# Performance work log

Measured on AMD Instinct MI355X. Metric: run time of the kernel, lower is better.

## Reference

```python
import jax, jax.numpy as jnp
import numpy as np
from jax import lax

B, C, H, W = 4, 64, 128, 128
G, K, CO = 8, 3, 64
KK = K * K
MC = G * KK  # mask channels = 72


def _conv3x3(x, w, b):
    # standard 3x3 conv, stride 1, padding 1, NCHW
    y = lax.conv_general_dilated(x, w, (1, 1), ((1, 1), (1, 1)),
                                 dimension_numbers=('NCHW', 'OIHW', 'NCHW'))
    return y + b[None, :, None, None]


def _deform_conv2d(x, offset, mask, w, b):
    """Modulated deformable conv (DCNv2), stride=1, padding=1, dilation=1.
    offset: [B, 2*G*KK, H, W] interpreted as [B, G, KK, 2(dy,dx), H, W] (torchvision layout).
    mask:   [B, G*KK, H, W].
    w: [Co, C/G, K, K], b: [Co].
    """
    Bn, Cn, Hn, Wn = x.shape
    Co, Cg, Kh, Kw = w.shape
    Gn = Cn // Cg
    KKn = Kh * Kw
    Ho, Wo = Hn, Wn  # stride 1, pad 1, k 3

    off = offset.reshape(Bn, Gn, KKn, 2, Ho, Wo)
    dy, dx = off[:, :, :, 0], off[:, :, :, 1]
    m = mask.reshape(Bn, Gn, 1, KKn, Ho, Wo)

    kh = (jnp.arange(KKn) // Kw).astype(x.dtype)  # kernel row index
    kw = (jnp.arange(KKn) % Kw).astype(x.dtype)
    hh = jnp.arange(Ho, dtype=x.dtype)
    ww = jnp.arange(Wo, dtype=x.dtype)
    # sampling positions: h - pad + kh*dil + dy  -> [B,G,KK,Ho,Wo]
    py = hh[None, None, None, :, None] - 1.0 + kh[None, None, :, None, None] + dy
    px = ww[None, None, None, None, :] - 1.0 + kw[None, None, :, None, None] + dx

    y0 = jnp.floor(py); x0 = jnp.floor(px)
    ly = py - y0; lx = px - x0
    y0i = y0.astype(jnp.int32); x0i = x0.astype(jnp.int32)
    y1i = y0i + 1; x1i = x0i + 1

    xg = x.reshape(Bn, Gn, Cg, Hn * Wn)

    def corner(yi, xi, wgt):
        valid = ((yi >= 0) & (yi < Hn) & (xi >= 0) & (xi < Wn)).astype(x.dtype)
        idx = (jnp.clip(yi, 0, Hn - 1) * Wn + jnp.clip(xi, 0, Wn - 1))
        idx = idx.reshape(Bn, Gn, 1, KKn * Ho * Wo)
        v = jnp.take_along_axis(xg, idx, axis=3).reshape(Bn, Gn, Cg, KKn, Ho, Wo)
        return v * (wgt * valid)[:, :, None]

    val = (corner(y0i, x0i, (1.0 - ly) * (1.0 - lx))
           + corner(y0i, x1i, (1.0 - ly) * lx)
           + corner(y1i, x0i, ly * (1.0 - lx))
           + corner(y1i, x1i, ly * lx))
    val = val * m  # modulation

    wr = w.reshape(Gn, Co // Gn, Cg, KKn)
    out = jnp.einsum('bgckhw,gock->bgohw', val, wr).reshape(Bn, Co, Ho, Wo)
    return out + b[None, :, None, None]


def setup_inputs() -> dict:
    key = jax.random.key(0)
    ks = jax.random.split(key, 8)
    f = lambda k, s, sc=1.0: jax.random.normal(k, s, dtype=jnp.float32) * sc
    return {
        'x': f(ks[0], (B, C, H, W)),
        'share_with_feat': f(ks[1], (B, C, H, W)),
        'offset_feat': f(ks[2], (B, C, H, W)),
        # conv_offset_mask: C -> 3*G*KK (zero-init in original; small random here)
        'w_om': f(ks[3], (3 * MC, C, 3, 3), 0.02),
        'b_om': jnp.zeros((3 * MC,), jnp.float32),
        'w_em1': f(ks[4], (C, 2 * C, 3, 3), 0.05),
        'b_em1': jnp.zeros((C,), jnp.float32),
        'w_em2': f(ks[5], (MC, C, 3, 3), 0.05),
        'b_em2': jnp.zeros((MC,), jnp.float32),
        # deform conv weight: [Co, C/G, 3, 3]
        'w_dc': f(ks[6], (CO, C // G, 3, 3), 0.05),
        'b_dc': f(ks[7], (CO,), 0.05),
    }


def reference(x, share_with_feat, offset_feat, w_om, b_om, w_em1, b_em1,
              w_em2, b_em2, w_dc, b_dc):
    om = _conv3x3(offset_feat, w_om, b_om)
    o1, o2, mask_x = jnp.split(om, 3, axis=1)
    offset = jnp.concatenate([o1, o2], axis=1)
    mask_x = jax.nn.sigmoid(mask_x)
    x_deform = _deform_conv2d(x, offset, mask_x, w_dc, b_dc)
    # extra_mask=True branch
    em = _conv3x3(jnp.concatenate([share_with_feat, offset_feat], axis=1), w_em1, b_em1)
    em = jnp.where(em >= 0, em, 0.1 * em)  # LeakyReLU(0.1)
    em = jax.nn.sigmoid(_conv3x3(em, w_em2, b_em2))
    share_deform = _deform_conv2d(share_with_feat, offset, em, w_dc, b_dc)
    return (x_deform, share_deform)
```

## Files before the change

kernel.cpp:

```cpp
#include <hip/hip_runtime.h>
#include <math.h>

#define BB 4
#define CC 64
#define HH 128
#define WW 128
#define GG 8
#define COO 64
#define HWC (HH*WW)

#define DPAD 12
#define DROW 26

typedef float f32x16 __attribute__((ext_vector_type(16)));
typedef __bf16 bf16x8 __attribute__((ext_vector_type(8)));

__device__ __forceinline__ unsigned short bf16_rn(float f) {
    unsigned int u = __float_as_uint(f);
    unsigned int r = (u + 0x7fffu + ((u >> 16) & 1u)) >> 16;
    return (unsigned short)r;
}
__device__ __forceinline__ float b2f(unsigned short u) {
    return __uint_as_float(((unsigned int)u) << 16);
}

__global__ __launch_bounds__(256) void pack_inputs_kernel(
    const float* __restrict__ x, const float* __restrict__ share,
    const float* __restrict__ offf,
    unsigned int* __restrict__ xs, unsigned short* __restrict__ sc16,
    unsigned short* __restrict__ oc16)
{
    __shared__ unsigned short lds[64][66];
    const int b = blockIdx.y;
    const int pix0 = blockIdx.x * 64;
    const int t = threadIdx.x;
    const int p = t & 63, q = t >> 6;
    const int pl = t & 63, cg = t >> 6;

#pragma unroll
    for (int i = 0; i < 16; i++) {
        int c = i * 4 + q;
        size_t idx = ((size_t)b * 64 + c) * HWC + pix0 + p;
        unsigned short sb = bf16_rn(share[idx]);
        lds[c][p] = sb;
        xs[idx] = (unsigned int)bf16_rn(x[idx]) | ((unsigned int)sb << 16);
    }
    __syncthreads();
    {
        unsigned int u[8];
#pragma unroll
        for (int j = 0; j < 8; j++) {
            unsigned int lo = lds[cg * 16 + 2 * j][pl];
            unsigned int hi = lds[cg * 16 + 2 * j + 1][pl];
            u[j] = lo | (hi << 16);
        }
        unsigned int* dst = (unsigned int*)(sc16 + ((size_t)(b * 4 + cg) * HWC + pix0 + pl) * 16);
        *(uint4*)dst = make_uint4(u[0], u[1], u[2], u[3]);
        *(uint4*)(dst + 4) = make_uint4(u[4], u[5], u[6], u[7]);
    }
    __syncthreads();

#pragma unroll
    for (int i = 0; i < 16; i++) {
        int c = i * 4 + q;
        lds[c][p] = bf16_rn(offf[((size_t)b * 64 + c) * HWC + pix0 + p]);
    }
    __syncthreads();
    {
        unsigned int u[8];
#pragma unroll
        for (int j = 0; j < 8; j++) {
            unsigned int lo = lds[cg * 16 + 2 * j][pl];
            unsigned int hi = lds[cg * 16 + 2 * j + 1][pl];
            u[j] = lo | (hi << 16);
        }
        unsigned int* dst = (unsigned int*)(oc16 + ((size_t)(b * 4 + cg) * HWC + pix0 + pl) * 16);
        *(uint4*)dst = make_uint4(u[0], u[1], u[2], u[3]);
        *(uint4*)(dst + 4) = make_uint4(u[4], u[5], u[6], u[7]);
    }
}

__device__ __forceinline__ void pack_w_one(const float* __restrict__ w,
                                           unsigned short* __restrict__ wp,
                                           int Cout, int COP, int CinTot, int idx) {
    int i  = idx & 15;
    int co = (idx >> 4) % COP;
    int t  = idx / (16 * COP);
    int cg = t & 3;
    int kk = (t >> 2) % 9;
    int seg = t / 36;
    int cin = seg * 64 + cg * 16 + i;
    float v = (co < Cout) ? w[((size_t)co * CinTot + cin) * 9 + kk] : 0.f;
    wp[idx] = bf16_rn(v);
}

__global__ void pack_w_all_kernel(const float* __restrict__ w_om, unsigned short* __restrict__ wp_om,
                                  const float* __restrict__ w_em1, unsigned short* __restrict__ wp_em1,
                                  const float* __restrict__ w_em2, unsigned short* __restrict__ wp_em2) {
    int i = blockIdx.x * 256 + threadIdx.x;
    if (i < 129024) {
        pack_w_one(w_om, wp_om, 216, 224, 64, i);
    } else if (i < 129024 + 73728) {
        pack_w_one(w_em1, wp_em1, 64, 64, 128, i - 129024);
    } else if (i < 129024 + 73728 + 55296) {
        pack_w_one(w_em2, wp_em2, 72, 96, 64, i - 129024 - 73728);
    }
}

template<int NSEG, int NT>
__global__ __launch_bounds__(256) void conv_mfma_kernel(
    const unsigned short* __restrict__ in0,
    const unsigned short* __restrict__ in1,
    const unsigned short* __restrict__ wp,
    const float* __restrict__ bias,
    void* __restrict__ out,
    int Cout, int COP, int out_mode, int act)
{
    constexpr int XS = 128 / (NT * 32);
    const int lane = threadIdx.x & 63;
    const int wid  = threadIdx.x >> 6;
    const int l31  = lane & 31;
    const int half = lane >> 5;
    int tmp = blockIdx.x;
    const int xsp = tmp % XS; tmp /= XS;
    const int rb  = tmp % (HH / 4);
    const int b   = tmp / (HH / 4);
    const int r   = rb * 4 + wid;
    const int px0 = xsp * NT * 32;
    const int co0 = blockIdx.y * 32;

    f32x16 acc[NT];
#pragma unroll
    for (int nt = 0; nt < NT; nt++)
#pragma unroll
        for (int rg = 0; rg < 16; rg++) acc[nt][rg] = 0.f;

    bf16x8 bz;
#pragma unroll
    for (int i = 0; i < 8; i++) bz[i] = (__bf16)0.f;

#pragma unroll
    for (int seg = 0; seg < NSEG; seg++) {
        const unsigned short* in = seg ? in1 : in0;
        const unsigned short* inb = in + (size_t)b * 4 * HWC * 16;
#pragma unroll
        for (int kk = 0; kk < 9; kk++) {
            const int rr = r + kk / 3 - 1;
            const bool rv = (unsigned)rr < (unsigned)HH;
            const int rrc = min(max(rr, 0), HH - 1);
            const int dxo = kk % 3 - 1;
#pragma unroll
            for (int cg = 0; cg < 4; cg++) {
                bf16x8 afrag = *(const bf16x8*)(wp +
                    ((size_t)(((seg * 9 + kk) * 4 + cg) * COP + co0 + l31) * 16 + half * 8));
                if (!rv) afrag = bz;
                const size_t plane = ((size_t)cg * HWC + (size_t)rrc * WW) * 16;
#pragma unroll
                for (int nt = 0; nt < NT; nt++) {
                    const int cc = px0 + nt * 32 + l31 + dxo;
                    bf16x8 bfrag = bz;
                    if ((unsigned)cc < (unsigned)WW)
                        bfrag = *(const bf16x8*)(inb + plane + (size_t)cc * 16 + half * 8);
                    acc[nt] = __builtin_amdgcn_mfma_f32_32x32x16_bf16(afrag, bfrag, acc[nt], 0, 0, 0);
                }
            }
        }
    }

#pragma unroll
    for (int nt = 0; nt < NT; nt++) {
#pragma unroll
        for (int rg = 0; rg < 16; rg++) {
            const int row = (rg & 3) + 8 * (rg >> 2) + 4 * half;
            const int co = co0 + row;
            if (co < Cout) {
                float v = acc[nt][rg] + bias[co];
                if (act == 1)      v = (v >= 0.f) ? v : 0.1f * v;
                else if (act == 2) v = 1.f / (1.f + __expf(-v));
                else if (act == 3 && co >= 144) v = 1.f / (1.f + __expf(-v));
                const int pix = r * WW + px0 + nt * 32 + l31;
                if (out_mode == 2)
                    ((unsigned short*)out)[((size_t)b * Cout + co) * HWC + pix] = bf16_rn(v);
                else
                    ((unsigned short*)out)[((size_t)(b * 4 + (co >> 4)) * HWC + pix) * 16 + (co & 15)] = bf16_rn(v);
            }
        }
    }
}

__global__ __launch_bounds__(256) void deform_fused_kernel(
    const unsigned int* __restrict__ xs,
    const unsigned short* __restrict__ om, const unsigned short* __restrict__ em,
    const float* __restrict__ wdc, const float* __restrict__ bdc,
    float* __restrict__ outx, float* __restrict__ outs)
{
    __shared__ __align__(16) unsigned int lds[24 * DROW * DPAD];

    const int bg = blockIdx.x >> 6;
    const int b = bg >> 3, g = bg & 7;
    const int tile = blockIdx.x & 63;
    const int r0 = (tile >> 3) << 4;
    const int c0 = (tile & 7) << 4;
    const int tx = threadIdx.x & 15, ty = threadIdx.x >> 4;
    const int h = r0 + ty, w = c0 + tx;
    const int wr0 = r0 - 4, wc0 = c0 - 4;

    const unsigned int* xsb = xs + ((size_t)b * 64 + g * 8) * HWC;

#pragma unroll
    for (int i = 0; i < 18; i++) {
        unsigned int slot = (unsigned int)threadIdx.x + i * 256u;
        unsigned int sx = slot % 24u;
        unsigned int t2 = slot / 24u;
        unsigned int sy = t2 % 24u;
        unsigned int c  = t2 / 24u;
        int iy = min(max(wr0 + (int)sy, 0), HH - 1);
        int ix = min(max(wc0 + (int)sx, 0), WW - 1);
        lds[(sy * DROW + sx) * DPAD + c] = xsb[(size_t)c * HWC + iy * WW + ix];
    }

    __syncthreads();

    const int pix = h * WW + w;
    const unsigned short* omb = om + (size_t)b * 216 * HWC + pix + (size_t)g * 18 * HWC;
    const unsigned short* mmb = om + (size_t)b * 216 * HWC + pix + (size_t)(144 + g * 9) * HWC;
    const unsigned short* emb = em + (size_t)b * 72 * HWC + pix + (size_t)g * 9 * HWC;

    float accx[8], accs[8];
#pragma unroll
    for (int o = 0; o < 8; o++) { accx[o] = 0.f; accs[o] = 0.f; }

#pragma unroll
    for (int kk = 0; kk < 9; kk++) {
        const float dy = b2f(omb[(size_t)(kk * 2) * HWC]);
        const float dx = b2f(omb[(size_t)(kk * 2 + 1) * HWC]);
        const float m1 = b2f(mmb[(size_t)kk * HWC]);
        const float m2 = b2f(emb[(size_t)kk * HWC]);

        const float py = (float)(h - 1 + kk / 3) + dy;
        const float px = (float)(w - 1 + kk % 3) + dx;
        const float y0f = floorf(py), x0f = floorf(px);
        const float ly = py - y0f, lx = px - x0f;
        const int y0 = (int)y0f, x0 = (int)x0f;
        const int y1 = y0 + 1, x1 = x0 + 1;
        const bool vy0 = (y0 >= 0) && (y0 < HH), vy1 = (y1 >= 0) && (y1 < HH);
        const bool vx0 = (x0 >= 0) && (x0 < WW), vx1 = (x1 >= 0) && (x1 < WW);
        float w00 = (1.f - ly) * (1.f - lx); if (!(vy0 && vx0)) w00 = 0.f;
        float w01 = (1.f - ly) * lx;         if (!(vy0 && vx1)) w01 = 0.f;
        float w10 = ly * (1.f - lx);         if (!(vy1 && vx0)) w10 = 0.f;
        float w11 = ly * lx;                 if (!(vy1 && vx1)) w11 = 0.f;
        const int cy0 = min(max(y0, 0), HH - 1), cy1 = min(max(y1, 0), HH - 1);
        const int cx0 = min(max(x0, 0), WW - 1), cx1 = min(max(x1, 0), WW - 1);

        const int sy0 = cy0 - wr0, sy1 = cy1 - wr0;
        const int sx0 = cx0 - wc0, sx1 = cx1 - wc0;
        const bool inw = (sy0 >= 0) && (sy1 < 24) && (sx0 >= 0) && (sx1 < 24);

        const float* wk = wdc + (size_t)g * 8 * 8 * 9 + kk;

        if (__builtin_expect(inw, 1)) {
            const int p00 = (sy0 * DROW + sx0) * DPAD, p01 = (sy0 * DROW + sx1) * DPAD;
            const int p10 = (sy1 * DROW + sx0) * DPAD, p11 = (sy1 * DROW + sx1) * DPAD;
#pragma unroll
            for (int ch = 0; ch < 2; ch++) {
                uint4 qa = *(const uint4*)(lds + p00 + ch * 4);
                uint4 qb = *(const uint4*)(lds + p01 + ch * 4);
                uint4 qc = *(const uint4*)(lds + p10 + ch * 4);
                uint4 qd = *(const uint4*)(lds + p11 + ch * 4);
                const unsigned int ua[4] = {qa.x, qa.y, qa.z, qa.w};
                const unsigned int ub[4] = {qb.x, qb.y, qb.z, qb.w};
                const unsigned int uc[4] = {qc.x, qc.y, qc.z, qc.w};
                const unsigned int ud[4] = {qd.x, qd.y, qd.z, qd.w};
#pragma unroll
                for (int j = 0; j < 4; j++) {
                    const int c = ch * 4 + j;
                    float x00 = __uint_as_float(ua[j] << 16), s00 = __uint_as_float(ua[j] & 0xffff0000u);
                    float x01 = __uint_as_float(ub[j] << 16), s01 = __uint_as_float(ub[j] & 0xffff0000u);
                    float x10 = __uint_as_float(uc[j] << 16), s10 = __uint_as_float(uc[j] & 0xffff0000u);
                    float x11 = __uint_as_float(ud[j] << 16), s11 = __uint_as_float(ud[j] & 0xffff0000u);
                    float vx = w00 * x00; vx = fmaf(w01, x01, vx); vx = fmaf(w10, x10, vx); vx = fmaf(w11, x11, vx);
                    float vs = w00 * s00; vs = fmaf(w01, s01, vs); vs = fmaf(w10, s10, vs); vs = fmaf(w11, s11, vs);
                    vx *= m1;
                    vs *= m2;
#pragma unroll
                    for (int o = 0; o < 8; o++) {
                        const float wv = wk[(size_t)(o * 8 + c) * 9];
                        accx[o] = fmaf(vx, wv, accx[o]);
                        accs[o] = fmaf(vs, wv, accs[o]);
                    }
                }
            }
        } else {
            const int i00 = cy0 * WW + cx0, i01 = cy0 * WW + cx1;
            const int i10 = cy1 * WW + cx0, i11 = cy1 * WW + cx1;
#pragma unroll
            for (int c = 0; c < 8; c++) {
                const unsigned int* xc = xsb + (size_t)c * HWC;
                unsigned int a = xc[i00], bq = xc[i01], cq = xc[i10], dq = xc[i11];
                float x00 = __uint_as_float(a << 16),  s00 = __uint_as_float(a & 0xffff0000u);
                float x01 = __uint_as_float(bq << 16), s01 = __uint_as_float(bq & 0xffff0000u);
                float x10 = __uint_as_float(cq << 16), s10 = __uint_as_float(cq & 0xffff0000u);
                float x11 = __uint_as_float(dq << 16), s11 = __uint_as_float(dq & 0xffff0000u);
                float vx = w00 * x00; vx = fmaf(w01, x01, vx); vx = fmaf(w10, x10, vx); vx = fmaf(w11, x11, vx);
                float vs = w00 * s00; vs = fmaf(w01, s01, vs); vs = fmaf(w10, s10, vs); vs = fmaf(w11, s11, vs);
                vx *= m1;
                vs *= m2;
#pragma unroll
                for (int o = 0; o < 8; o++) {
                    const float wv = wk[(size_t)(o * 8 + c) * 9];
                    accx[o] = fmaf(vx, wv, accx[o]);
                    accs[o] = fmaf(vs, wv, accs[o]);
                }
            }
        }
    }

#pragma unroll
    for (int o = 0; o < 8; o++) {
        const float bv = bdc[g * 8 + o];
        outx[((size_t)(b * COO + g * 8 + o)) * HWC + pix] = accx[o] + bv;
        outs[((size_t)(b * COO + g * 8 + o)) * HWC + pix] = accs[o] + bv;
    }
}

extern "C" void kernel_launch(void* const* d_in, const int* in_sizes, int n_in,
                              void* d_out, int out_size, void* d_ws, size_t ws_size,
                              hipStream_t stream) {
    const float* x      = (const float*)d_in[0];
    const float* share  = (const float*)d_in[1];
    const float* offf   = (const float*)d_in[2];
    const float* w_om   = (const float*)d_in[3];
    const float* b_om   = (const float*)d_in[4];
    const float* w_em1  = (const float*)d_in[5];
    const float* b_em1  = (const float*)d_in[6];
    const float* w_em2  = (const float*)d_in[7];
    const float* b_em2  = (const float*)d_in[8];
    const float* w_dc   = (const float*)d_in[9];
    const float* b_dc   = (const float*)d_in[10];

    unsigned int* xs = (unsigned int*)d_ws;
    unsigned short* us = (unsigned short*)(xs + 4194304);
    unsigned short* sc16   = us;
    unsigned short* oc16   = sc16 + 4194304;
    unsigned short* emm    = oc16 + 4194304;
    unsigned short* om_b   = emm + 4194304;
    unsigned short* em_b   = om_b + 14155776;
    unsigned short* wp_om  = em_b + 4718592;
    unsigned short* wp_em1 = wp_om + 129024;
    unsigned short* wp_em2 = wp_em1 + 73728;

    float* outx = (float*)d_out;
    float* outs = outx + 4194304;

    dim3 blk(256);

    pack_inputs_kernel<<<dim3(HWC / 64, BB), blk, 0, stream>>>(x, share, offf, xs, sc16, oc16);
    pack_w_all_kernel<<<(258048 + 255) / 256, blk, 0, stream>>>(
        w_om, wp_om, w_em1, wp_em1, w_em2, wp_em2);

    conv_mfma_kernel<1, 2><<<dim3(BB * (HH / 4) * 2, 7), blk, 0, stream>>>(
        oc16, nullptr, wp_om, b_om, om_b, 216, 224, 2, 3);
    conv_mfma_kernel<2, 1><<<dim3(BB * (HH / 4) * 4, 2), blk, 0, stream>>>(
        sc16, oc16, wp_em1, b_em1, emm, 64, 64, 3, 1);
    conv_mfma_kernel<1, 1><<<dim3(BB * (HH / 4) * 4, 3), blk, 0, stream>>>(
        emm, nullptr, wp_em2, b_em2, em_b, 72, 96, 2, 2);

    deform_fused_kernel<<<dim3(BB * GG * 64), blk, 0, stream>>>(
        xs, om_b, em_b, w_dc, b_dc, outx, outs);
}
```

Baseline: 276.1 us.

## Stage conv input rows in LDS and tile output channels per wave

Each conv block now handles one full output row. It loads the three needed input rows (with halo, zero-padded) into shared memory once, and each wave computes 32 pixels across several 32-channel output tiles. Before, each wave read input fragments straight from global memory for every output-channel tile. The change raises input reuse across output channels, and the om weight padding grows to 256 channels. It adds an LDS staging pass and barriers, cuts the block count, and raises register use for multiple accumulators.

```diff
diff --git a/kernel.cpp b/kernel.cpp
--- a/kernel.cpp
+++ b/kernel.cpp
@@ -98,16 +98,16 @@
                                   const float* __restrict__ w_em1, unsigned short* __restrict__ wp_em1,
                                   const float* __restrict__ w_em2, unsigned short* __restrict__ wp_em2) {
     int i = blockIdx.x * 256 + threadIdx.x;
-    if (i < 129024) {
-        pack_w_one(w_om, wp_om, 216, 224, 64, i);
-    } else if (i < 129024 + 73728) {
-        pack_w_one(w_em1, wp_em1, 64, 64, 128, i - 129024);
-    } else if (i < 129024 + 73728 + 55296) {
-        pack_w_one(w_em2, wp_em2, 72, 96, 64, i - 129024 - 73728);
-    }
-}
-
-template<int NSEG, int NT>
+    if (i < 147456) {
+        pack_w_one(w_om, wp_om, 216, 256, 64, i);
+    } else if (i < 147456 + 73728) {
+        pack_w_one(w_em1, wp_em1, 64, 64, 128, i - 147456);
+    } else if (i < 147456 + 73728 + 55296) {
+        pack_w_one(w_em2, wp_em2, 72, 96, 64, i - 147456 - 73728);
+    }
+}
+
+template<int NSEG, int MB>
 __global__ __launch_bounds__(256) void conv_mfma_kernel(
     const unsigned short* __restrict__ in0,
     const unsigned short* __restrict__ in1,
@@ -116,69 +116,78 @@
     void* __restrict__ out,
     int Cout, int COP, int out_mode, int act)
 {
-    constexpr int XS = 128 / (NT * 32);
+    __shared__ __align__(16) unsigned short smem[4 * 3 * 132 * 16];
+
     const int lane = threadIdx.x & 63;
     const int wid  = threadIdx.x >> 6;
     const int l31  = lane & 31;
     const int half = lane >> 5;
-    int tmp = blockIdx.x;
-    const int xsp = tmp % XS; tmp /= XS;
-    const int rb  = tmp % (HH / 4);
-    const int b   = tmp / (HH / 4);
-    const int r   = rb * 4 + wid;
-    const int px0 = xsp * NT * 32;
-    const int co0 = blockIdx.y * 32;
-
-    f32x16 acc[NT];
-#pragma unroll
-    for (int nt = 0; nt < NT; nt++)
-#pragma unroll
-        for (int rg = 0; rg < 16; rg++) acc[nt][rg] = 0.f;
-
-    bf16x8 bz;
-#pragma unroll
-    for (int i = 0; i < 8; i++) bz[i] = (__bf16)0.f;
+    const int b    = blockIdx.x >> 7;
+    const int r    = blockIdx.x & (HH - 1);
+    const int coB  = blockIdx.y * (MB * 32);
+
+    f32x16 acc[MB];
+#pragma unroll
+    for (int mb = 0; mb < MB; mb++)
+#pragma unroll
+        for (int rg = 0; rg < 16; rg++) acc[mb][rg] = 0.f;
 
 #pragma unroll
     for (int seg = 0; seg < NSEG; seg++) {
         const unsigned short* in = seg ? in1 : in0;
         const unsigned short* inb = in + (size_t)b * 4 * HWC * 16;
+
+        if (seg > 0) __syncthreads();
+        for (int i = threadIdx.x; i < 1584; i += 256) {
+            int pxs = i % 132;
+            int t2  = i / 132;
+            int ri  = t2 % 3, cg = t2 / 3;
+            int rr  = r + ri - 1;
+            int px  = pxs - 2;
+            uint4 lo = make_uint4(0, 0, 0, 0), hi = make_uint4(0, 0, 0, 0);
+            if ((unsigned)rr < (unsigned)HH && (unsigned)px < (unsigned)WW) {
+                const unsigned short* src = inb + ((size_t)cg * HWC + rr * WW + px) * 16;
+                lo = *(const uint4*)src;
+                hi = *(const uint4*)(src + 8);
+            }
+            unsigned short* d = smem + ((size_t)(cg * 3 + ri) * 132 + pxs) * 16;
+            *(uint4*)d = lo;
+            *(uint4*)(d + 8) = hi;
+        }
+        __syncthreads();
+
 #pragma unroll
         for (int kk = 0; kk < 9; kk++) {
-            const int rr = r + kk / 3 - 1;
-            const bool rv = (unsigned)rr < (unsigned)HH;
-            const int rrc = min(max(rr, 0), HH - 1);
+            const int ri = kk / 3;
             const int dxo = kk % 3 - 1;
 #pragma unroll
             for (int cg = 0; cg < 4; cg++) {
-                bf16x8 afrag = *(const bf16x8*)(wp +
-                    ((size_t)(((seg * 9 + kk) * 4 + cg) * COP + co0 + l31) * 16 + half * 8));
-                if (!rv) afrag = bz;
-                const size_t plane = ((size_t)cg * HWC + (size_t)rrc * WW) * 16;
-#pragma unroll
-                for (int nt = 0; nt < NT; nt++) {
-                    const int cc = px0 + nt * 32 + l31 + dxo;
-                    bf16x8 bfrag = bz;
-                    if ((unsigned)cc < (unsigned)WW)
-                        bfrag = *(const bf16x8*)(inb + plane + (size_t)cc * 16 + half * 8);
-                    acc[nt] = __builtin_amdgcn_mfma_f32_32x32x16_bf16(afrag, bfrag, acc[nt], 0, 0, 0);
+                bf16x8 bfrag = *(const bf16x8*)(smem +
+                    ((size_t)(cg * 3 + ri) * 132 + (wid * 32 + l31 + dxo + 2)) * 16 + half * 8);
+                const unsigned short* wrow = wp +
+                    (size_t)(((seg * 9 + kk) * 4 + cg)) * COP * 16;
+#pragma unroll
+                for (int mb = 0; mb < MB; mb++) {
+                    bf16x8 afrag = *(const bf16x8*)(wrow +
+                        (size_t)(coB + mb * 32 + l31) * 16 + half * 8);
+                    acc[mb] = __builtin_amdgcn_mfma_f32_32x32x16_bf16(afrag, bfrag, acc[mb], 0, 0, 0);
                 }
             }
         }
     }
 
 #pragma unroll
-    for (int nt = 0; nt < NT; nt++) {
+    for (int mb = 0; mb < MB; mb++) {
 #pragma unroll
         for (int rg = 0; rg < 16; rg++) {
             const int row = (rg & 3) + 8 * (rg >> 2) + 4 * half;
-            const int co = co0 + row;
+            const int co = coB + mb * 32 + row;
             if (co < Cout) {
-                float v = acc[nt][rg] + bias[co];
+                float v = acc[mb][rg] + bias[co];
                 if (act == 1)      v = (v >= 0.f) ? v : 0.1f * v;
                 else if (act == 2) v = 1.f / (1.f + __expf(-v));
                 else if (act == 3 && co >= 144) v = 1.f / (1.f + __expf(-v));
-                const int pix = r * WW + px0 + nt * 32 + l31;
+                const int pix = r * WW + wid * 32 + l31;
                 if (out_mode == 2)
                     ((unsigned short*)out)[((size_t)b * Cout + co) * HWC + pix] = bf16_rn(v);
                 else
@@ -346,7 +355,7 @@
     unsigned short* om_b   = emm + 4194304;
     unsigned short* em_b   = om_b + 14155776;
     unsigned short* wp_om  = em_b + 4718592;
-    unsigned short* wp_em1 = wp_om + 129024;
+    unsigned short* wp_em1 = wp_om + 147456;
     unsigned short* wp_em2 = wp_em1 + 73728;
 
     float* outx = (float*)d_out;
@@ -355,14 +364,14 @@
     dim3 blk(256);
 
     pack_inputs_kernel<<<dim3(HWC / 64, BB), blk, 0, stream>>>(x, share, offf, xs, sc16, oc16);
-    pack_w_all_kernel<<<(258048 + 255) / 256, blk, 0, stream>>>(
+    pack_w_all_kernel<<<(276480 + 255) / 256, blk, 0, stream>>>(
         w_om, wp_om, w_em1, wp_em1, w_em2, wp_em2);
 
-    conv_mfma_kernel<1, 2><<<dim3(BB * (HH / 4) * 2, 7), blk, 0, stream>>>(
-        oc16, nullptr, wp_om, b_om, om_b, 216, 224, 2, 3);
-    conv_mfma_kernel<2, 1><<<dim3(BB * (HH / 4) * 4, 2), blk, 0, stream>>>(
+    conv_mfma_kernel<1, 4><<<dim3(BB * HH, 2), blk, 0, stream>>>(
+        oc16, nullptr, wp_om, b_om, om_b, 216, 256, 2, 3);
+    conv_mfma_kernel<2, 2><<<dim3(BB * HH, 1), blk, 0, stream>>>(
         sc16, oc16, wp_em1, b_em1, emm, 64, 64, 3, 1);
-    conv_mfma_kernel<1, 1><<<dim3(BB * (HH / 4) * 4, 3), blk, 0, stream>>>(
+    conv_mfma_kernel<1, 3><<<dim3(BB * HH, 1), blk, 0, stream>>>(
         emm, nullptr, wp_em2, b_em2, em_b, 72, 96, 2, 2);
 
     deform_fused_kernel<<<dim3(BB * GG * 64), blk, 0, stream>>>(
```

Result: slower. 300.9 us (+9.0%).
